# Kernel optimization log

Hardware: AMD Instinct MI355X
Metric: run time of the kernel (lower is better)

The kernel has to match this reference:

```python
import jax, jax.numpy as jnp
import numpy as np

NUM_BASES = 32   # cfg.MODEL.FCPOSE.BASIS_MODULE.NUM_BASES
CH = 32          # cfg.MODEL.FCPOSE.DYNAMIC_CHANNELS
NKP = 17         # keypoints
STRIDE = 8       # base_stride
ATTN_LEN = (2 + NUM_BASES) * CH + CH + CH * CH + CH + CH * NKP + NKP  # 2737


def setup_inputs() -> dict:
    key = jax.random.key(0)
    ks = jax.random.split(key, 6)
    n_inst, H, W = 64, 100, 152
    bases_full = jax.random.normal(ks[0], (1, NUM_BASES + 2 * NKP, H, W), jnp.float32)
    top_feats = jax.random.normal(ks[1], (n_inst, 256 * 9), jnp.float32)
    # proposal locations in input-image pixel coords
    locations = jax.random.uniform(ks[2], (n_inst, 2), jnp.float32) * jnp.array([W * STRIDE, H * STRIDE], jnp.float32)
    atten_W = jax.random.normal(ks[3], (ATTN_LEN, 256 * 9), jnp.float32) * 0.01
    atten_b = jnp.zeros((ATTN_LEN,), jnp.float32)
    sizes_of_interest = jnp.array([64.0, 128.0, 256.0, 512.0, 1333.0], jnp.float32)
    fpn_levels = jax.random.randint(ks[4], (n_inst,), 0, 5)
    return dict(bases_full=bases_full, top_feats=top_feats, locations=locations,
                atten_W=atten_W, atten_b=atten_b,
                sizes_of_interest=sizes_of_interest, fpn_levels=fpn_levels)


def reference(bases_full, top_feats, locations, atten_W, atten_b, sizes_of_interest, fpn_levels):
    _, C, H, W = bases_full.shape
    HW = H * W
    n_inst = top_feats.shape[0]

    # compute_locations_per_level (stride 8, +stride//2 offset)
    sx = jnp.arange(W, dtype=jnp.float32) * STRIDE + STRIDE // 2
    sy = jnp.arange(H, dtype=jnp.float32) * STRIDE + STRIDE // 2
    gx, gy = jnp.meshgrid(sx, sy)                      # each [H, W]
    base_locs = jnp.stack([gx.reshape(-1), gy.reshape(-1)], axis=1)  # [HW, 2]

    bases = bases_full[0, :NUM_BASES]                  # [nb, H, W]
    dirmap = bases_full[0, NUM_BASES:]                 # [34, H, W]
    # direction = direction + per-pixel (x, y) location tiled per keypoint
    dirmap = dirmap + jnp.tile(jnp.stack([gx, gy], axis=0), (NKP, 1, 1))

    # per-instance normalized offsets
    max_ranges = sizes_of_interest[fpn_levels]                             # [n]
    off = (locations[:, None, :] - base_locs[None, :, :]).transpose(0, 2, 1)  # [n, 2, HW]
    off = off / max_ranges[:, None, None]
    x0 = jnp.concatenate(
        [off, jnp.broadcast_to(bases.reshape(1, NUM_BASES, HW), (n_inst, NUM_BASES, HW))],
        axis=1)                                                             # [n, 2+nb, HW]

    # dynamic subnetwork params from linear atten_producer
    attns = top_feats @ atten_W.T + atten_b            # [n, 2737]
    sizes = [(2 + NUM_BASES) * CH, CH, CH * CH, CH, CH * NKP, NKP]
    w0, b0, w1, b1, w2, b2 = jnp.split(attns, np.cumsum(sizes)[:-1], axis=1)
    w0 = w0.reshape(n_inst, CH, 2 + NUM_BASES)
    w1 = w1.reshape(n_inst, CH, CH)
    w2 = w2.reshape(n_inst, NKP, CH)

    # grouped 1x1 convs == per-instance small matmuls over pixels
    h = jax.nn.relu(jnp.einsum('noc,nci->noi', w0, x0) + b0[:, :, None])
    h = jax.nn.relu(jnp.einsum('noc,nci->noi', w1, h) + b1[:, :, None])
    logits = jnp.einsum('noc,nci->noi', w2, h) + b2[:, :, None]   # [n, 17, HW]

    # inference head: argmax over pixels, gather predicted direction as keypoint
    idx = jnp.argmax(logits, axis=2)                                # [n, 17]
    dir_flat = dirmap.reshape(NKP, 2, HW).transpose(0, 2, 1)        # [17, HW, 2]
    pred_keypoints = dir_flat[jnp.arange(NKP)[None, :], idx]        # [n, 17, 2]

    return logits.reshape(n_inst, NKP, H, W), pred_keypoints
```

## Files before the change

### kernel.cpp

```cpp
#include <hip/hip_runtime.h>
#include <stdint.h>

constexpr int NBASES = 32;
constexpr int NKP    = 17;
constexpr int HDIM   = 100, WDIM = 152;
constexpr int HW     = HDIM * WDIM;
constexpr int NI     = 64;
constexpr int KF     = 2304;
constexpr int AL     = 2737;
constexpr int ALP    = 2740;
constexpr int OB0 = 1088;
constexpr int OW1 = 1120;
constexpr int OB1 = 2144;
constexpr int OW2 = 2176;
constexpr int OB2 = 2720;
constexpr int TW0 = 0;
constexpr int TB0 = 1088;
constexpr int TW1 = 1120;
constexpr int TB1 = 2144;
constexpr int TW2 = 2176;
constexpr int TB2 = 2720;

constexpr int PXB = 512;
constexpr int NBX = (HW + PXB - 1) / PXB;

constexpr int JT     = 64;
constexpr int KCH    = 64;
constexpr int KSPLIT = 12;
constexpr int KT     = KF / KSPLIT;
constexpr int NJT    = (AL + JT - 1) / JT;
constexpr int JTOT   = NJT * JT;
constexpr int LPAD   = 68;

constexpr size_t ATT_OFF   = 0;
constexpr size_t ARGP_OFF  = (size_t)NI * ALP * 4;
constexpr size_t GEMMP_OFF = ARGP_OFF + (size_t)NI * NKP * NBX * 8;

__device__ __forceinline__ int perm(int j) {
    if (j < OB0)      { int o = j / 34, c = j - o * 34; return TW0 + c * 32 + o; }
    else if (j < OW1) return TB0 + (j - OB0);
    else if (j < OB1) { int q = j - OW1; int o = q >> 5, c = q & 31; return TW1 + c * 32 + o; }
    else if (j < OW2) return TB1 + (j - OB1);
    else if (j < OB2) return TW2 + (j - OW2);
    else              return TB2 + (j - OB2);
}

__global__ __launch_bounds__(256) void gemm_attn(const float* __restrict__ tf,
                                                 const float* __restrict__ W,
                                                 float* __restrict__ partial) {
    __shared__ __align__(16) float Tl[KCH][LPAD];
    __shared__ __align__(16) float Wl[KCH][LPAD];
    int jb = blockIdx.x % NJT;
    int ks = blockIdx.x / NJT;
    int j0 = jb * JT;
    int k0 = ks * KT;
    int tid = threadIdx.x;
    int tn = tid % 16;
    int tj = tid / 16;
    int lk = tid % 64;
    int lr = tid / 64;
    float acc[4][4] = {};
    for (int kc = 0; kc < KT; kc += KCH) {
        int kbase = k0 + kc;
        #pragma unroll
        for (int i = 0; i < 16; i++) {
            int nn = lr * 16 + i;
            Tl[lk][nn] = tf[(size_t)nn * KF + kbase + lk];
        }
        #pragma unroll
        for (int i = 0; i < 16; i++) {
            int j = j0 + lr * 16 + i;
            Wl[lk][lr * 16 + i] = (j < AL) ? W[(size_t)j * KF + kbase + lk] : 0.0f;
        }
        __syncthreads();
        #pragma unroll 4
        for (int kk = 0; kk < KCH; ++kk) {
            float tv[4], wv[4];
            #pragma unroll
            for (int i = 0; i < 4; i++) tv[i] = Tl[kk][tn * 4 + i];
            #pragma unroll
            for (int i = 0; i < 4; i++) wv[i] = Wl[kk][tj * 4 + i];
            #pragma unroll
            for (int i = 0; i < 4; i++)
                #pragma unroll
                for (int q = 0; q < 4; q++) acc[i][q] += tv[i] * wv[q];
        }
        __syncthreads();
    }
    size_t pbase = (size_t)(ks * NI) * JTOT;
    #pragma unroll
    for (int i = 0; i < 4; i++) {
        int nn = tn * 4 + i;
        int j = j0 + tj * 4;
        float4 st = make_float4(acc[i][0], acc[i][1], acc[i][2], acc[i][3]);
        *(float4*)&partial[pbase + (size_t)nn * JTOT + j] = st;
    }
}

__global__ __launch_bounds__(256) void reduce_attn(const float* __restrict__ partial,
                                                   const float* __restrict__ b,
                                                   float* __restrict__ att_p) {
    int n = blockIdx.y;
    int j = blockIdx.x * 256 + threadIdx.x;
    if (j >= AL) return;
    float s = b[j];
    #pragma unroll
    for (int ks = 0; ks < KSPLIT; ks++)
        s += partial[(size_t)(ks * NI + n) * JTOT + j];
    att_p[(size_t)n * ALP + perm(j)] = s;
}

constexpr int LB0 = 1088;
constexpr int LB1 = 1120;
constexpr int LW2 = 1152;
constexpr int LB2 = 1696;
constexpr int LTOT = 1716;

__device__ inline unsigned int mono_f32(float f) {
    unsigned int u = __float_as_uint(f);
    return (u & 0x80000000u) ? ~u : (u | 0x80000000u);
}

__global__ __launch_bounds__(256) void pixel_head(const float* __restrict__ bases_full,
                                                  const float* __restrict__ att_p,
                                                  const float* __restrict__ locations,
                                                  const float* __restrict__ soi,
                                                  const int* __restrict__ fpn,
                                                  float* __restrict__ out_logits,
                                                  unsigned long long* __restrict__ partial) {
    __shared__ __align__(16) float w[LTOT];
    __shared__ unsigned long long red[4][NKP];
    int n = blockIdx.y, bx = blockIdx.x, tid = threadIdx.x;
    const float* wn = att_p + (size_t)n * ALP;

    {
        const float4* s4 = (const float4*)wn;
        float4* d4 = (float4*)w;
        for (int i = tid; i < 280; i += 256) d4[i] = s4[i];
        if (tid < 149) d4[280 + tid] = s4[536 + tid];
    }
    __syncthreads();

    int p0 = bx * PXB + tid * 2;
    bool valid = p0 < HW;
    int pc = valid ? p0 : 0;
    int y = pc / WDIM, x = pc - y * WDIM;

    float inv = 1.0f / soi[fpn[n]];
    float lx = locations[2 * n], ly = locations[2 * n + 1];
    float cxa = (lx - (float)(x * 8 + 4)) * inv;
    float cxb = (lx - (float)(x * 8 + 12)) * inv;
    float cyy = (ly - (float)(y * 8 + 4)) * inv;

    float ha[32], hb[32];
    {
        const float4* br  = (const float4*)&w[LB0];
        const float4* w0r = (const float4*)&w[TW0];
        const float4* w1r = (const float4*)&w[TW0 + 32];
        #pragma unroll
        for (int g = 0; g < 8; g++) {
            float4 b4 = br[g], wv = w0r[g], wu = w1r[g];
            ha[4*g+0] = b4.x + wv.x * cxa + wu.x * cyy;  hb[4*g+0] = b4.x + wv.x * cxb + wu.x * cyy;
            ha[4*g+1] = b4.y + wv.y * cxa + wu.y * cyy;  hb[4*g+1] = b4.y + wv.y * cxb + wu.y * cyy;
            ha[4*g+2] = b4.z + wv.z * cxa + wu.z * cyy;  hb[4*g+2] = b4.z + wv.z * cxb + wu.z * cyy;
            ha[4*g+3] = b4.w + wv.w * cxa + wu.w * cyy;  hb[4*g+3] = b4.w + wv.w * cxb + wu.w * cyy;
        }
    }
    #pragma unroll 4
    for (int c = 0; c < 32; c++) {
        float2 bv = *(const float2*)&bases_full[(size_t)c * HW + pc];
        const float4* wr = (const float4*)&w[TW0 + (c + 2) * 32];
        #pragma unroll
        for (int g = 0; g < 8; g++) {
            float4 wv = wr[g];
            ha[4*g+0] += wv.x * bv.x;  hb[4*g+0] += wv.x * bv.y;
            ha[4*g+1] += wv.y * bv.x;  hb[4*g+1] += wv.y * bv.y;
            ha[4*g+2] += wv.z * bv.x;  hb[4*g+2] += wv.z * bv.y;
            ha[4*g+3] += wv.w * bv.x;  hb[4*g+3] += wv.w * bv.y;
        }
    }
    #pragma unroll
    for (int o = 0; o < 32; o++) {
        ha[o] = fmaxf(ha[o], 0.0f);
        hb[o] = fmaxf(hb[o], 0.0f);
    }

    float ga[32], gb[32];
    {
        const float4* br = (const float4*)&w[LB1];
        #pragma unroll
        for (int g = 0; g < 8; g++) {
            float4 b4 = br[g];
            ga[4*g+0] = b4.x; ga[4*g+1] = b4.y; ga[4*g+2] = b4.z; ga[4*g+3] = b4.w;
        }
        #pragma unroll
        for (int o = 0; o < 32; o++) gb[o] = ga[o];
    }
    #pragma unroll 4
    for (int c = 0; c < 32; c++) {
        float xa = ha[c], xb = hb[c];
        const float4* wr = (const float4*)(wn + TW1 + c * 32);
        #pragma unroll
        for (int g = 0; g < 8; g++) {
            float4 wv = wr[g];
            ga[4*g+0] += wv.x * xa;  gb[4*g+0] += wv.x * xb;
            ga[4*g+1] += wv.y * xa;  gb[4*g+1] += wv.y * xb;
            ga[4*g+2] += wv.z * xa;  gb[4*g+2] += wv.z * xb;
            ga[4*g+3] += wv.w * xa;  gb[4*g+3] += wv.w * xb;
        }
    }
    #pragma unroll
    for (int o = 0; o < 32; o++) {
        ga[o] = fmaxf(ga[o], 0.0f);
        gb[o] = fmaxf(gb[o], 0.0f);
    }

    size_t obase = (size_t)n * NKP * HW;
    int wid = tid >> 6, lane = tid & 63;
    #pragma unroll
    for (int k = 0; k < NKP; k++) {
        const float4* wr = (const float4*)&w[LW2 + k * 32];
        float sa = w[LB2 + k], sb = sa;
        #pragma unroll
        for (int g = 0; g < 8; g++) {
            float4 wv = wr[g];
            sa += wv.x * ga[4*g+0] + wv.y * ga[4*g+1] + wv.z * ga[4*g+2] + wv.w * ga[4*g+3];
            sb += wv.x * gb[4*g+0] + wv.y * gb[4*g+1] + wv.z * gb[4*g+2] + wv.w * gb[4*g+3];
        }
        unsigned long long pk = 0;
        if (valid) {
            *(float2*)&out_logits[obase + (size_t)k * HW + p0] = make_float2(sa, sb);
            float bv = sa; int bp = p0;
            if (sb > sa) { bv = sb; bp = p0 + 1; }
            pk = ((unsigned long long)mono_f32(bv) << 32) |
                 (unsigned long long)(0xFFFFFFFFu - (unsigned)bp);
        }
        #pragma unroll
        for (int off = 32; off > 0; off >>= 1) {
            unsigned long long o = __shfl_down(pk, off);
            if (o > pk) pk = o;
        }
        if (lane == 0) red[wid][k] = pk;
    }
    __syncthreads();
    if (tid < NKP) {
        unsigned long long m = red[0][tid];
        #pragma unroll
        for (int ww = 1; ww < 4; ww++)
            if (red[ww][tid] > m) m = red[ww][tid];
        partial[((size_t)n * NKP + tid) * NBX + bx] = m;
    }
}

__global__ __launch_bounds__(64) void kp_final(const unsigned long long* __restrict__ partial,
                                               const float* __restrict__ bases_full,
                                               float* __restrict__ kp_out) {
    int b = blockIdx.x;
    int n = b / NKP, k = b % NKP;
    int lane = threadIdx.x;
    unsigned long long v = (lane < NBX) ? partial[((size_t)n * NKP + k) * NBX + lane] : 0ull;
    #pragma unroll
    for (int off = 32; off > 0; off >>= 1) {
        unsigned long long o = __shfl_down(v, off);
        if (o > v) v = o;
    }
    if (lane == 0) {
        int p = (int)(0xFFFFFFFFu - (unsigned)(v & 0xFFFFFFFFull));
        int yy = p / WDIM;
        int xx = p - yy * WDIM;
        float kx = bases_full[(size_t)(NBASES + 2 * k) * HW + p] + (float)(xx * 8 + 4);
        float ky = bases_full[(size_t)(NBASES + 2 * k + 1) * HW + p] + (float)(yy * 8 + 4);
        kp_out[((size_t)n * NKP + k) * 2 + 0] = kx;
        kp_out[((size_t)n * NKP + k) * 2 + 1] = ky;
    }
}

extern "C" void kernel_launch(void* const* d_in, const int* in_sizes, int n_in,
                              void* d_out, int out_size, void* d_ws, size_t ws_size,
                              hipStream_t stream) {
    const float* bases_full = (const float*)d_in[0];
    const float* top_feats  = (const float*)d_in[1];
    const float* locations  = (const float*)d_in[2];
    const float* atten_W    = (const float*)d_in[3];
    const float* atten_b    = (const float*)d_in[4];
    const float* soi        = (const float*)d_in[5];
    const int*   fpn        = (const int*)d_in[6];
    float* out   = (float*)d_out;
    float* att_p = (float*)((char*)d_ws + ATT_OFF);
    unsigned long long* argp = (unsigned long long*)((char*)d_ws + ARGP_OFF);
    float* gemmp = (float*)((char*)d_ws + GEMMP_OFF);

    gemm_attn<<<NJT * KSPLIT, 256, 0, stream>>>(top_feats, atten_W, gemmp);

    dim3 gr((AL + 255) / 256, NI);
    reduce_attn<<<gr, 256, 0, stream>>>(gemmp, atten_b, att_p);

    dim3 g2(NBX, NI);
    pixel_head<<<g2, 256, 0, stream>>>(bases_full, att_p, locations, soi, fpn, out, argp);

    float* kp_out = out + (size_t)NI * NKP * HW;
    kp_final<<<NI * NKP, 64, 0, stream>>>(argp, bases_full, kp_out);
}
```

Before: 232.8 us.

## Process one pixel per thread with 512-thread blocks and prefetched base loads

The pixel head now has each thread handle one pixel instead of two, with 512 threads per block (PXB unchanged). This roughly halves the register arrays and raises occupancy under launch_bounds(512,4). All dynamic weights, including w1 which was previously read from global memory, are now staged in shared memory. Base-channel loads are software-prefetched four channels ahead, and logits are written with nontemporal stores. The cost is more threads per pixel, so each thread gets less weight reuse from every LDS read, and the reduction now spans 8 waves.

```diff
diff --git a/kernel.cpp b/kernel.cpp
--- a/kernel.cpp
+++ b/kernel.cpp
@@ -110,130 +110,126 @@
     att_p[(size_t)n * ALP + perm(j)] = s;
 }
 
-constexpr int LB0 = 1088;
-constexpr int LB1 = 1120;
-constexpr int LW2 = 1152;
-constexpr int LB2 = 1696;
-constexpr int LTOT = 1716;
-
 __device__ inline unsigned int mono_f32(float f) {
     unsigned int u = __float_as_uint(f);
     return (u & 0x80000000u) ? ~u : (u | 0x80000000u);
 }
 
-__global__ __launch_bounds__(256) void pixel_head(const float* __restrict__ bases_full,
-                                                  const float* __restrict__ att_p,
-                                                  const float* __restrict__ locations,
-                                                  const float* __restrict__ soi,
-                                                  const int* __restrict__ fpn,
-                                                  float* __restrict__ out_logits,
-                                                  unsigned long long* __restrict__ partial) {
-    __shared__ __align__(16) float w[LTOT];
-    __shared__ unsigned long long red[4][NKP];
+__global__ __launch_bounds__(512, 4) void pixel_head(const float* __restrict__ bases_full,
+                                                     const float* __restrict__ att_p,
+                                                     const float* __restrict__ locations,
+                                                     const float* __restrict__ soi,
+                                                     const int* __restrict__ fpn,
+                                                     float* __restrict__ out_logits,
+                                                     unsigned long long* __restrict__ partial) {
+    __shared__ __align__(16) float w[ALP];
+    __shared__ unsigned long long red[8][NKP];
     int n = blockIdx.y, bx = blockIdx.x, tid = threadIdx.x;
     const float* wn = att_p + (size_t)n * ALP;
 
     {
         const float4* s4 = (const float4*)wn;
         float4* d4 = (float4*)w;
-        for (int i = tid; i < 280; i += 256) d4[i] = s4[i];
-        if (tid < 149) d4[280 + tid] = s4[536 + tid];
+        for (int i = tid; i < ALP / 4; i += 512) d4[i] = s4[i];
     }
     __syncthreads();
 
-    int p0 = bx * PXB + tid * 2;
+    int p0 = bx * PXB + tid;
     bool valid = p0 < HW;
     int pc = valid ? p0 : 0;
     int y = pc / WDIM, x = pc - y * WDIM;
 
     float inv = 1.0f / soi[fpn[n]];
     float lx = locations[2 * n], ly = locations[2 * n + 1];
-    float cxa = (lx - (float)(x * 8 + 4)) * inv;
-    float cxb = (lx - (float)(x * 8 + 12)) * inv;
-    float cyy = (ly - (float)(y * 8 + 4)) * inv;
-
-    float ha[32], hb[32];
+    float cx = (lx - (float)(x * 8 + 4)) * inv;
+    float cy = (ly - (float)(y * 8 + 4)) * inv;
+
+    const float* bp = bases_full + pc;
+    float q0 = bp[0], q1 = bp[HW], q2 = bp[2 * (size_t)HW], q3 = bp[3 * (size_t)HW];
+
+    float h[32];
     {
-        const float4* br  = (const float4*)&w[LB0];
+        const float4* br  = (const float4*)&w[TB0];
         const float4* w0r = (const float4*)&w[TW0];
         const float4* w1r = (const float4*)&w[TW0 + 32];
         #pragma unroll
         for (int g = 0; g < 8; g++) {
             float4 b4 = br[g], wv = w0r[g], wu = w1r[g];
-            ha[4*g+0] = b4.x + wv.x * cxa + wu.x * cyy;  hb[4*g+0] = b4.x + wv.x * cxb + wu.x * cyy;
-            ha[4*g+1] = b4.y + wv.y * cxa + wu.y * cyy;  hb[4*g+1] = b4.y + wv.y * cxb + wu.y * cyy;
-            ha[4*g+2] = b4.z + wv.z * cxa + wu.z * cyy;  hb[4*g+2] = b4.z + wv.z * cxb + wu.z * cyy;
-            ha[4*g+3] = b4.w + wv.w * cxa + wu.w * cyy;  hb[4*g+3] = b4.w + wv.w * cxb + wu.w * cyy;
+            h[4*g+0] = b4.x + wv.x * cx + wu.x * cy;
+            h[4*g+1] = b4.y + wv.y * cx + wu.y * cy;
+            h[4*g+2] = b4.z + wv.z * cx + wu.z * cy;
+            h[4*g+3] = b4.w + wv.w * cx + wu.w * cy;
+        }
+    }
+    #pragma unroll
+    for (int c0 = 0; c0 < 32; c0 += 4) {
+        float n0 = 0.f, n1 = 0.f, n2 = 0.f, n3 = 0.f;
+        if (c0 + 4 < 32) {
+            n0 = bp[(size_t)(c0 + 4) * HW];
+            n1 = bp[(size_t)(c0 + 5) * HW];
+            n2 = bp[(size_t)(c0 + 6) * HW];
+            n3 = bp[(size_t)(c0 + 7) * HW];
+        }
+        float qq[4] = {q0, q1, q2, q3};
+        #pragma unroll
+        for (int u = 0; u < 4; u++) {
+            float bv = qq[u];
+            const float4* wr = (const float4*)&w[TW0 + (c0 + u + 2) * 32];
+            #pragma unroll
+            for (int g = 0; g < 8; g++) {
+                float4 wv = wr[g];
+                h[4*g+0] += wv.x * bv;
+                h[4*g+1] += wv.y * bv;
+                h[4*g+2] += wv.z * bv;
+                h[4*g+3] += wv.w * bv;
+            }
+        }
+        q0 = n0; q1 = n1; q2 = n2; q3 = n3;
+    }
+    #pragma unroll
+    for (int o = 0; o < 32; o++) h[o] = fmaxf(h[o], 0.0f);
+
+    float gg[32];
+    {
+        const float4* br = (const float4*)&w[TB1];
+        #pragma unroll
+        for (int g = 0; g < 8; g++) {
+            float4 b4 = br[g];
+            gg[4*g+0] = b4.x; gg[4*g+1] = b4.y; gg[4*g+2] = b4.z; gg[4*g+3] = b4.w;
         }
     }
     #pragma unroll 4
     for (int c = 0; c < 32; c++) {
-        float2 bv = *(const float2*)&bases_full[(size_t)c * HW + pc];
-        const float4* wr = (const float4*)&w[TW0 + (c + 2) * 32];
+        float xv = h[c];
+        const float4* wr = (const float4*)&w[TW1 + c * 32];
         #pragma unroll
         for (int g = 0; g < 8; g++) {
             float4 wv = wr[g];
-            ha[4*g+0] += wv.x * bv.x;  hb[4*g+0] += wv.x * bv.y;
-            ha[4*g+1] += wv.y * bv.x;  hb[4*g+1] += wv.y * bv.y;
-            ha[4*g+2] += wv.z * bv.x;  hb[4*g+2] += wv.z * bv.y;
-            ha[4*g+3] += wv.w * bv.x;  hb[4*g+3] += wv.w * bv.y;
-        }
-    }
-    #pragma unroll
-    for (int o = 0; o < 32; o++) {
-        ha[o] = fmaxf(ha[o], 0.0f);
-        hb[o] = fmaxf(hb[o], 0.0f);
-    }
-
-    float ga[32], gb[32];
-    {
-        const float4* br = (const float4*)&w[LB1];
-        #pragma unroll
-        for (int g = 0; g < 8; g++) {
-            float4 b4 = br[g];
-            ga[4*g+0] = b4.x; ga[4*g+1] = b4.y; ga[4*g+2] = b4.z; ga[4*g+3] = b4.w;
-        }
-        #pragma unroll
-        for (int o = 0; o < 32; o++) gb[o] = ga[o];
-    }
-    #pragma unroll 4
-    for (int c = 0; c < 32; c++) {
-        float xa = ha[c], xb = hb[c];
-        const float4* wr = (const float4*)(wn + TW1 + c * 32);
-        #pragma unroll
-        for (int g = 0; g < 8; g++) {
-            float4 wv = wr[g];
-            ga[4*g+0] += wv.x * xa;  gb[4*g+0] += wv.x * xb;
-            ga[4*g+1] += wv.y * xa;  gb[4*g+1] += wv.y * xb;
-            ga[4*g+2] += wv.z * xa;  gb[4*g+2] += wv.z * xb;
-            ga[4*g+3] += wv.w * xa;  gb[4*g+3] += wv.w * xb;
-        }
-    }
-    #pragma unroll
-    for (int o = 0; o < 32; o++) {
-        ga[o] = fmaxf(ga[o], 0.0f);
-        gb[o] = fmaxf(gb[o], 0.0f);
-    }
+            gg[4*g+0] += wv.x * xv;
+            gg[4*g+1] += wv.y * xv;
+            gg[4*g+2] += wv.z * xv;
+            gg[4*g+3] += wv.w * xv;
+        }
+    }
+    #pragma unroll
+    for (int o = 0; o < 32; o++) gg[o] = fmaxf(gg[o], 0.0f);
 
     size_t obase = (size_t)n * NKP * HW;
     int wid = tid >> 6, lane = tid & 63;
     #pragma unroll
     for (int k = 0; k < NKP; k++) {
-        const float4* wr = (const float4*)&w[LW2 + k * 32];
-        float sa = w[LB2 + k], sb = sa;
+        const float4* wr = (const float4*)&w[TW2 + k * 32];
+        float s = w[TB2 + k];
         #pragma unroll
         for (int g = 0; g < 8; g++) {
             float4 wv = wr[g];
-            sa += wv.x * ga[4*g+0] + wv.y * ga[4*g+1] + wv.z * ga[4*g+2] + wv.w * ga[4*g+3];
-            sb += wv.x * gb[4*g+0] + wv.y * gb[4*g+1] + wv.z * gb[4*g+2] + wv.w * gb[4*g+3];
+            s += wv.x * gg[4*g+0] + wv.y * gg[4*g+1] + wv.z * gg[4*g+2] + wv.w * gg[4*g+3];
         }
         unsigned long long pk = 0;
         if (valid) {
-            *(float2*)&out_logits[obase + (size_t)k * HW + p0] = make_float2(sa, sb);
-            float bv = sa; int bp = p0;
-            if (sb > sa) { bv = sb; bp = p0 + 1; }
-            pk = ((unsigned long long)mono_f32(bv) << 32) |
-                 (unsigned long long)(0xFFFFFFFFu - (unsigned)bp);
+            __builtin_nontemporal_store(s, &out_logits[obase + (size_t)k * HW + p0]);
+            pk = ((unsigned long long)mono_f32(s) << 32) |
+                 (unsigned long long)(0xFFFFFFFFu - (unsigned)p0);
         }
         #pragma unroll
         for (int off = 32; off > 0; off >>= 1) {
@@ -246,7 +242,7 @@
     if (tid < NKP) {
         unsigned long long m = red[0][tid];
         #pragma unroll
-        for (int ww = 1; ww < 4; ww++)
+        for (int ww = 1; ww < 8; ww++)
             if (red[ww][tid] > m) m = red[ww][tid];
         partial[((size_t)n * NKP + tid) * NBX + bx] = m;
     }
@@ -296,7 +292,7 @@
     reduce_attn<<<gr, 256, 0, stream>>>(gemmp, atten_b, att_p);
 
     dim3 g2(NBX, NI);
-    pixel_head<<<g2, 256, 0, stream>>>(bases_full, att_p, locations, soi, fpn, out, argp);
+    pixel_head<<<g2, 512, 0, stream>>>(bases_full, att_p, locations, soi, fpn, out, argp);
 
     float* kp_out = out + (size_t)NI * NKP * HW;
     kp_final<<<NI * NKP, 64, 0, stream>>>(argp, bases_full, kp_out);
```

Measured after the change: 264.2 us. 1.14x slower.
